# Performance work log

Measured on AMD Instinct MI355X. Metric: run time of the kernel, lower is better.

## Reference

```python
import jax, jax.numpy as jnp
import numpy as np

B, N, C, T = 2048, 512, 64, 128  # batch, codebook size, latent channels, latent time


def setup_inputs() -> dict:
    key = jax.random.key(0)
    k1, k2 = jax.random.split(key)
    y = jax.random.normal(k1, (B, C, T), dtype=jnp.float32)   # encoder latents
    m = jax.random.normal(k2, (N, C, T), dtype=jnp.float32)   # centroid means
    sd = jnp.ones((N, C, T), dtype=jnp.float32)               # centroid variances
    p = jnp.zeros((N,), dtype=jnp.float32) + 1e-6             # cluster counts
    return {"y": y, "m": m, "sd": sd, "p": p}


def reference(y, m, sd, p):
    # --- squared-distance argmin assignment (same math as (y-m)^2 summed over C,T) ---
    b = y.shape[0]
    yf = y.reshape(b, -1)                 # [B, D]
    mf = m.reshape(m.shape[0], -1)        # [N, D]
    d2 = (yf * yf).sum(-1)[:, None] + (mf * mf).sum(-1)[None, :] - 2.0 * (yf @ mf.T)
    assign = jnp.argmin(d2, axis=1)       # [B] int assignments

    # --- sequential, order-sensitive EMA scatter updates (faithful to python loop) ---
    def step(carry, inp):
        p_, m_, sd_ = carry
        yi, zi = inp
        p_ = p_.at[zi].add(1.0)
        mi = m_[zi] * 0.001 + yi * 0.999
        m_ = m_.at[zi].set(mi)
        sdi = (mi - yi) ** 2 * 0.001 + sd_[zi] * 0.999
        sd_ = sd_.at[zi].set(sdi)
        return (p_, m_, sd_), None

    (p, m, sd), _ = jax.lax.scan(step, (p, m, sd), (y, assign))
    return m, sd, p, assign
```

## Files before the change

### kernel.cpp

```cpp
#include <hip/hip_runtime.h>
#include <hip/hip_bf16.h>


#define Bb 2048
#define Nn 512
#define Dd 8192
#define MARGIN 12.0f
#define KC 8
#define KSTEPS 32

typedef __attribute__((ext_vector_type(4))) float f32x4;
typedef __attribute__((ext_vector_type(8))) short s16x8;

__device__ inline unsigned pack2(float lo, float hi) {
    return __builtin_amdgcn_perm(__float_as_uint(hi), __float_as_uint(lo), 0x07060302u);
}

__device__ inline void ema4(float4& mcv, float4& scv, const float4 yv) {
#define EMA_C(c) { mcv.c = mcv.c * 0.001f + yv.c * 0.999f; \
                   float d_ = mcv.c - yv.c;                 \
                   scv.c = d_ * d_ * 0.001f + scv.c * 0.999f; }
    EMA_C(x) EMA_C(y) EMA_C(z) EMA_C(w)
#undef EMA_C
}

__global__ __launch_bounds__(256) void m_norms(const float* __restrict__ M,
                                               float* __restrict__ mm) {
    int n = blockIdx.x, t = threadIdx.x;
    const float4* r = (const float4*)(M + (size_t)n * Dd);
    float s = 0.f;
#pragma unroll
    for (int u = 0; u < 8; u++) {
        float4 v = r[t + 256 * u];
        s += v.x * v.x + v.y * v.y + v.z * v.z + v.w * v.w;
    }
    __shared__ float red[256];
    red[t] = s;
    __syncthreads();
    for (int off = 128; off > 0; off >>= 1) {
        if (t < off) red[t] += red[t + off];
        __syncthreads();
    }
    if (t == 0) mm[n] = red[0];
}

__global__ __launch_bounds__(512, 4) void gemm_coarse(const float* __restrict__ Y,
                                                      const float* __restrict__ M,
                                                      float* __restrict__ part) {
    __shared__ __align__(16) unsigned short As[2][128 * 32];
    __shared__ __align__(16) unsigned short Bs[2][128 * 32];
    const int t = threadIdx.x;
    const int lane = t & 63;
    const int w = t >> 6;

    const int bid = blockIdx.x;
    const int kc = bid & 7;
    const int ct = (bid >> 3) & 3;
    const int rt = bid >> 5;

    const size_t ybase = (size_t)rt * 128 * Dd + (size_t)kc * (KSTEPS * 32);
    const size_t mbase = (size_t)ct * 128 * Dd + (size_t)kc * (KSTEPS * 32);

    const int rowT = t >> 2;
    const int segT = t & 3;
    const int dstOff = rowT * 32 + (segT ^ ((rowT >> 1) & 3)) * 8;
    const float* gA0 = Y + ybase + (size_t)rowT * Dd + segT * 8;
    const float* gB0 = M + mbase + (size_t)rowT * Dd + segT * 8;

    const int wr0 = (w & 3) * 32, wc0 = (w >> 2) * 64;
    const int l15 = lane & 15, quad = lane >> 4;

    f32x4 acc[2][4];
#pragma unroll
    for (int i = 0; i < 2; i++)
#pragma unroll
        for (int j = 0; j < 4; j++) acc[i][j] = (f32x4)(0.0f);

    float4 ra0, ra1, rb0, rb1;
    auto loads = [&](int step) {
        const float* pa = gA0 + step * 32;
        const float* pb = gB0 + step * 32;
        ra0 = *(const float4*)pa;  ra1 = *(const float4*)(pa + 4);
        rb0 = *(const float4*)pb;  rb1 = *(const float4*)(pb + 4);
    };
    auto writes = [&](int buf) {
        union { unsigned u[4]; s16x8 s; } pa_, pb_;
        pa_.u[0] = pack2(ra0.x, ra0.y);  pa_.u[1] = pack2(ra0.z, ra0.w);
        pa_.u[2] = pack2(ra1.x, ra1.y);  pa_.u[3] = pack2(ra1.z, ra1.w);
        pb_.u[0] = pack2(rb0.x, rb0.y);  pb_.u[1] = pack2(rb0.z, rb0.w);
        pb_.u[2] = pack2(rb1.x, rb1.y);  pb_.u[3] = pack2(rb1.z, rb1.w);
        *(s16x8*)(&As[buf][dstOff]) = pa_.s;
        *(s16x8*)(&Bs[buf][dstOff]) = pb_.s;
    };
    auto compute = [&](int buf) {
        s16x8 fa[2], fb[4];
#pragma unroll
        for (int ta = 0; ta < 2; ta++) {
            int rowa = wr0 + ta * 16 + l15;
            int sega = quad ^ ((rowa >> 1) & 3);
            fa[ta] = *(const s16x8*)(&As[buf][rowa * 32 + sega * 8]);
        }
#pragma unroll
        for (int tb = 0; tb < 4; tb++) {
            int rowb = wc0 + tb * 16 + l15;
            int segb = quad ^ ((rowb >> 1) & 3);
            fb[tb] = *(const s16x8*)(&Bs[buf][rowb * 32 + segb * 8]);
        }
#pragma unroll
        for (int i = 0; i < 2; i++)
#pragma unroll
            for (int j = 0; j < 4; j++)
                acc[i][j] = __builtin_amdgcn_mfma_f32_16x16x32_bf16(fa[i], fb[j], acc[i][j], 0, 0, 0);
    };

    loads(0);
    writes(0);
    __syncthreads();
    for (int step = 0; step < KSTEPS; step++) {
        const int buf = step & 1;
        if (step + 1 < KSTEPS) loads(step + 1);
        compute(buf);
        if (step + 1 < KSTEPS) writes(buf ^ 1);
        __syncthreads();
    }

    float* P = part + (size_t)kc * (Bb * Nn);
#pragma unroll
    for (int i = 0; i < 2; i++) {
        int rg = rt * 128 + wr0 + i * 16 + quad * 4;
#pragma unroll
        for (int j = 0; j < 4; j++) {
            int cg = ct * 128 + wc0 + j * 16 + l15;
#pragma unroll
            for (int r = 0; r < 4; r++)
                P[(size_t)(rg + r) * Nn + cg] = acc[i][j][r];
        }
    }
}

__global__ __launch_bounds__(256) void rescore(const float* __restrict__ Y,
                                               const float* __restrict__ M,
                                               const float* __restrict__ part,
                                               const float* __restrict__ mm,
                                               float* __restrict__ assignF) {
    __shared__ float redW[4];
    __shared__ int candList[Nn];
    __shared__ float candD2[Nn];
    __shared__ int candCnt;
    int b = blockIdx.x, t = threadIdx.x, lane = t & 63, w = t >> 6;
    if (t == 0) candCnt = 0;

    int c0 = t, c1 = t + 256;
    float dot0 = 0.f, dot1 = 0.f;
#pragma unroll
    for (int k = 0; k < KC; k++) {
        dot0 += part[(size_t)k * (Bb * Nn) + (size_t)b * Nn + c0];
        dot1 += part[(size_t)k * (Bb * Nn) + (size_t)b * Nn + c1];
    }
    float d0 = mm[c0] - 2.0f * dot0;
    float d1 = mm[c1] - 2.0f * dot1;

    float mn = fminf(d0, d1);
#pragma unroll
    for (int off = 32; off > 0; off >>= 1) mn = fminf(mn, __shfl_xor(mn, off));
    if (lane == 0) redW[w] = mn;
    __syncthreads();
    float thresh = fminf(fminf(redW[0], redW[1]), fminf(redW[2], redW[3])) + MARGIN;

    if (d0 <= thresh) candList[atomicAdd(&candCnt, 1)] = c0;
    if (d1 <= thresh) candList[atomicAdd(&candCnt, 1)] = c1;
    __syncthreads();
    int ncand = candCnt;

    if (ncand == 1) {
        if (t == 0) assignF[b] = (float)candList[0];
        return;
    }

    const float4* yr = (const float4*)(Y + (size_t)b * Dd);
    for (int j = w; j < ncand; j += 4) {
        int c = candList[j];
        const float4* mr = (const float4*)(M + (size_t)c * Dd);
        float p = 0.f;
#pragma unroll 8
        for (int u = 0; u < 32; u++) {
            float4 yv = yr[u * 64 + lane];
            float4 mv = mr[u * 64 + lane];
            p += yv.x * mv.x + yv.y * mv.y + yv.z * mv.z + yv.w * mv.w;
        }
#pragma unroll
        for (int off = 32; off > 0; off >>= 1) p += __shfl_xor(p, off);
        if (lane == 0) candD2[j] = mm[c] - 2.0f * p;
    }
    __syncthreads();

    if (t == 0) {
        float bestV = 3.4e38f;
        int bestI = 0x3fffffff;
        for (int j = 0; j < ncand; j++) {
            float d2e = candD2[j];
            int c = candList[j];
            if (d2e < bestV || (d2e == bestV && c < bestI)) { bestV = d2e; bestI = c; }
        }
        assignF[b] = (float)bestI;
    }
}

__global__ __launch_bounds__(256) void ema_scatter(const float* __restrict__ Y,
                                                   const float* __restrict__ M0,
                                                   const float* __restrict__ SD0,
                                                   const float* __restrict__ P0,
                                                   const float* __restrict__ assignF,
                                                   float* __restrict__ m_out,
                                                   float* __restrict__ sd_out,
                                                   float* __restrict__ p_out) {
    __shared__ int lst[Bb];
    __shared__ int cnt4[4];
    int n = blockIdx.x, s = blockIdx.y, t = threadIdx.x, lane = t & 63, w = t >> 6;

    int eqf[8], myidx[8];
    int cntW = 0;
#pragma unroll
    for (int k = 0; k < 8; k++) {
        int u = w * 8 + k;
        int zi = (int)assignF[u * 64 + lane];
        int eq = (zi == n) ? 1 : 0;
        unsigned long long mask = __ballot(eq != 0);
        eqf[k] = eq;
        myidx[k] = cntW + (int)__popcll(mask & ((1ull << lane) - 1ull));
        cntW += (int)__popcll(mask);
    }
    if (lane == 0) cnt4[w] = cntW;
    __syncthreads();
    int off0 = 0;
#pragma unroll
    for (int q = 0; q < 4; q++) off0 += (q < w) ? cnt4[q] : 0;
    int cnt = cnt4[0] + cnt4[1] + cnt4[2] + cnt4[3];
#pragma unroll
    for (int k = 0; k < 8; k++)
        if (eqf[k]) lst[off0 + myidx[k]] = (w * 8 + k) * 64 + lane;
    if (t == 0 && s == 0) p_out[n] = P0[n] + (float)cnt;
    __syncthreads();

    size_t off = (size_t)n * Dd + (size_t)s * 1024;
    float4 mc = *(const float4*)(M0 + off + 4 * t);
    float4 sc = *(const float4*)(SD0 + off + 4 * t);

    int j = 0;
    for (; j + 16 <= cnt; j += 16) {
        float4 yv[16];
#pragma unroll
        for (int q = 0; q < 16; q++)
            yv[q] = *(const float4*)(Y + (size_t)lst[j + q] * Dd + (size_t)s * 1024 + 4 * t);
#pragma unroll
        for (int q = 0; q < 16; q++) ema4(mc, sc, yv[q]);
    }
    for (; j + 4 <= cnt; j += 4) {
        float4 yv[4];
#pragma unroll
        for (int q = 0; q < 4; q++)
            yv[q] = *(const float4*)(Y + (size_t)lst[j + q] * Dd + (size_t)s * 1024 + 4 * t);
#pragma unroll
        for (int q = 0; q < 4; q++) ema4(mc, sc, yv[q]);
    }
    for (; j < cnt; j++) {
        float4 yv = *(const float4*)(Y + (size_t)lst[j] * Dd + (size_t)s * 1024 + 4 * t);
        ema4(mc, sc, yv);
    }

    *(float4*)(m_out + off + 4 * t) = mc;
    *(float4*)(sd_out + off + 4 * t) = sc;
}

extern "C" void kernel_launch(void* const* d_in, const int* in_sizes, int n_in,
                              void* d_out, int out_size, void* d_ws, size_t ws_size,
                              hipStream_t stream) {
    const float* y  = (const float*)d_in[0];
    const float* m  = (const float*)d_in[1];
    const float* sd = (const float*)d_in[2];
    const float* p  = (const float*)d_in[3];

    float* out     = (float*)d_out;
    float* m_out   = out;
    float* sd_out  = out + 4194304;
    float* p_out   = out + 8388608;
    float* assignF = out + 8389120;
    float* part    = out;

    m_norms    <<<Nn, 256, 0, stream>>>(m, p_out);
    gemm_coarse<<<dim3(512), 512, 0, stream>>>(y, m, part);
    rescore    <<<Bb, 256, 0, stream>>>(y, m, part, p_out, assignF);
    ema_scatter<<<dim3(Nn, 8), 256, 0, stream>>>(y, m, sd, p, assignF, m_out, sd_out, p_out);
}
```

Before: 209.4 us.

## Prefetch two K-steps ahead in coarse GEMM with coalesced row-split loads

The coarse bf16 GEMM now keeps two sets of prefetch registers, so global loads run two K-steps ahead of the MFMA compute instead of one. The global-to-LDS mapping also changes: each thread loads a float4 from two rows 64 apart, giving 128-byte contiguous row segments per 8 threads, and writes 8-byte bf16 stores with no XOR swizzle. The aim is to hide more global latency and improve coalescing. The cost is more registers, possible LDS bank conflicts on the now unswizzled fragment reads, and narrower LDS stores.

```diff
diff --git a/kernel.cpp b/kernel.cpp
--- a/kernel.cpp
+++ b/kernel.cpp
@@ -11,9 +11,17 @@
 
 typedef __attribute__((ext_vector_type(4))) float f32x4;
 typedef __attribute__((ext_vector_type(8))) short s16x8;
+typedef __attribute__((ext_vector_type(2))) unsigned u32x2;
 
 __device__ inline unsigned pack2(float lo, float hi) {
     return __builtin_amdgcn_perm(__float_as_uint(hi), __float_as_uint(lo), 0x07060302u);
+}
+
+__device__ inline void st4bf(unsigned short* dst, const float4 v) {
+    u32x2 x;
+    x[0] = pack2(v.x, v.y);
+    x[1] = pack2(v.z, v.w);
+    *(u32x2*)dst = x;
 }
 
 __device__ inline void ema4(float4& mcv, float4& scv, const float4 yv) {
@@ -61,11 +69,11 @@
     const size_t ybase = (size_t)rt * 128 * Dd + (size_t)kc * (KSTEPS * 32);
     const size_t mbase = (size_t)ct * 128 * Dd + (size_t)kc * (KSTEPS * 32);
 
-    const int rowT = t >> 2;
-    const int segT = t & 3;
-    const int dstOff = rowT * 32 + (segT ^ ((rowT >> 1) & 3)) * 8;
-    const float* gA0 = Y + ybase + (size_t)rowT * Dd + segT * 8;
-    const float* gB0 = M + mbase + (size_t)rowT * Dd + segT * 8;
+    const int rL = t >> 3;
+    const int g4 = (t & 7) * 4;
+    const float* gA0 = Y + ybase + (size_t)rL * Dd + g4;
+    const float* gB0 = M + mbase + (size_t)rL * Dd + g4;
+    const int dst0 = rL * 32 + g4;
 
     const int wr0 = (w & 3) * 32, wc0 = (w >> 2) * 64;
     const int l15 = lane & 15, quad = lane >> 4;
@@ -76,36 +84,42 @@
 #pragma unroll
         for (int j = 0; j < 4; j++) acc[i][j] = (f32x4)(0.0f);
 
-    float4 ra0, ra1, rb0, rb1;
-    auto loads = [&](int step) {
+    float4 aA0, aA1, aB0, aB1;
+    float4 bA0, bA1, bB0, bB1;
+    const size_t rowskip = (size_t)64 * Dd;
+
+    auto loadsA = [&](int step) {
         const float* pa = gA0 + step * 32;
         const float* pb = gB0 + step * 32;
-        ra0 = *(const float4*)pa;  ra1 = *(const float4*)(pa + 4);
-        rb0 = *(const float4*)pb;  rb1 = *(const float4*)(pb + 4);
-    };
-    auto writes = [&](int buf) {
-        union { unsigned u[4]; s16x8 s; } pa_, pb_;
-        pa_.u[0] = pack2(ra0.x, ra0.y);  pa_.u[1] = pack2(ra0.z, ra0.w);
-        pa_.u[2] = pack2(ra1.x, ra1.y);  pa_.u[3] = pack2(ra1.z, ra1.w);
-        pb_.u[0] = pack2(rb0.x, rb0.y);  pb_.u[1] = pack2(rb0.z, rb0.w);
-        pb_.u[2] = pack2(rb1.x, rb1.y);  pb_.u[3] = pack2(rb1.z, rb1.w);
-        *(s16x8*)(&As[buf][dstOff]) = pa_.s;
-        *(s16x8*)(&Bs[buf][dstOff]) = pb_.s;
+        aA0 = *(const float4*)pa;  aA1 = *(const float4*)(pa + rowskip);
+        aB0 = *(const float4*)pb;  aB1 = *(const float4*)(pb + rowskip);
+    };
+    auto loadsB = [&](int step) {
+        const float* pa = gA0 + step * 32;
+        const float* pb = gB0 + step * 32;
+        bA0 = *(const float4*)pa;  bA1 = *(const float4*)(pa + rowskip);
+        bB0 = *(const float4*)pb;  bB1 = *(const float4*)(pb + rowskip);
+    };
+    auto writesA = [&](int buf) {
+        st4bf(&As[buf][dst0],        aA0);
+        st4bf(&As[buf][dst0 + 2048], aA1);
+        st4bf(&Bs[buf][dst0],        aB0);
+        st4bf(&Bs[buf][dst0 + 2048], aB1);
+    };
+    auto writesB = [&](int buf) {
+        st4bf(&As[buf][dst0],        bA0);
+        st4bf(&As[buf][dst0 + 2048], bA1);
+        st4bf(&Bs[buf][dst0],        bB0);
+        st4bf(&Bs[buf][dst0 + 2048], bB1);
     };
     auto compute = [&](int buf) {
         s16x8 fa[2], fb[4];
 #pragma unroll
-        for (int ta = 0; ta < 2; ta++) {
-            int rowa = wr0 + ta * 16 + l15;
-            int sega = quad ^ ((rowa >> 1) & 3);
-            fa[ta] = *(const s16x8*)(&As[buf][rowa * 32 + sega * 8]);
-        }
-#pragma unroll
-        for (int tb = 0; tb < 4; tb++) {
-            int rowb = wc0 + tb * 16 + l15;
-            int segb = quad ^ ((rowb >> 1) & 3);
-            fb[tb] = *(const s16x8*)(&Bs[buf][rowb * 32 + segb * 8]);
-        }
+        for (int ta = 0; ta < 2; ta++)
+            fa[ta] = *(const s16x8*)(&As[buf][(wr0 + ta * 16 + l15) * 32 + quad * 8]);
+#pragma unroll
+        for (int tb = 0; tb < 4; tb++)
+            fb[tb] = *(const s16x8*)(&Bs[buf][(wc0 + tb * 16 + l15) * 32 + quad * 8]);
 #pragma unroll
         for (int i = 0; i < 2; i++)
 #pragma unroll
@@ -113,14 +127,18 @@
                 acc[i][j] = __builtin_amdgcn_mfma_f32_16x16x32_bf16(fa[i], fb[j], acc[i][j], 0, 0, 0);
     };
 
-    loads(0);
-    writes(0);
-    __syncthreads();
-    for (int step = 0; step < KSTEPS; step++) {
-        const int buf = step & 1;
-        if (step + 1 < KSTEPS) loads(step + 1);
-        compute(buf);
-        if (step + 1 < KSTEPS) writes(buf ^ 1);
+    loadsA(0);
+    loadsB(1);
+    writesA(0);
+    __syncthreads();
+    for (int step = 0; step < KSTEPS; step += 2) {
+        if (step + 2 < KSTEPS) loadsA(step + 2);
+        compute(0);
+        writesB(1);
+        __syncthreads();
+        if (step + 3 < KSTEPS) loadsB(step + 3);
+        compute(1);
+        if (step + 2 < KSTEPS) writesA(0);
         __syncthreads();
     }
 
```

Result: no change. 212.7 us (+1.6%).

## Double K tile depth to 64 in coarse GEMM with new swizzle and lighter barrier

Applied to the files above, without the earlier changes.

Doubles the K-slice per pipeline step from 32 to 64 and halves the step count, so each block runs half as many barriers and buffer swaps. Global loads are reorganised into 16-byte chunks across two row halves, stored to LDS as 8-byte bf16 pairs under an XOR swizzle over 8 blocks. __syncthreads is replaced by an explicit lgkmcnt wait plus s_barrier, which skips waiting on outstanding global loads. LDS use doubles to 64KB per block, which may cut occupancy under the 512x4 launch bound, and the narrower LDS stores may raise store instruction count.

```diff
diff --git a/kernel.cpp b/kernel.cpp
--- a/kernel.cpp
+++ b/kernel.cpp
@@ -7,13 +7,22 @@
 #define Dd 8192
 #define MARGIN 12.0f
 #define KC 8
-#define KSTEPS 32
+#define KSTEPS 16
+#define BK 64
 
 typedef __attribute__((ext_vector_type(4))) float f32x4;
 typedef __attribute__((ext_vector_type(8))) short s16x8;
+typedef __attribute__((ext_vector_type(2))) unsigned u32x2;
 
 __device__ inline unsigned pack2(float lo, float hi) {
     return __builtin_amdgcn_perm(__float_as_uint(hi), __float_as_uint(lo), 0x07060302u);
+}
+
+__device__ inline void st4bf(unsigned short* dst, const float4 v) {
+    u32x2 x;
+    x[0] = pack2(v.x, v.y);
+    x[1] = pack2(v.z, v.w);
+    *(u32x2*)dst = x;
 }
 
 __device__ inline void ema4(float4& mcv, float4& scv, const float4 yv) {
@@ -47,8 +56,8 @@
 __global__ __launch_bounds__(512, 4) void gemm_coarse(const float* __restrict__ Y,
                                                       const float* __restrict__ M,
                                                       float* __restrict__ part) {
-    __shared__ __align__(16) unsigned short As[2][128 * 32];
-    __shared__ __align__(16) unsigned short Bs[2][128 * 32];
+    __shared__ __align__(16) unsigned short As[2][128 * BK];
+    __shared__ __align__(16) unsigned short Bs[2][128 * BK];
     const int t = threadIdx.x;
     const int lane = t & 63;
     const int w = t >> 6;
@@ -58,14 +67,16 @@
     const int ct = (bid >> 3) & 3;
     const int rt = bid >> 5;
 
-    const size_t ybase = (size_t)rt * 128 * Dd + (size_t)kc * (KSTEPS * 32);
-    const size_t mbase = (size_t)ct * 128 * Dd + (size_t)kc * (KSTEPS * 32);
-
-    const int rowT = t >> 2;
-    const int segT = t & 3;
-    const int dstOff = rowT * 32 + (segT ^ ((rowT >> 1) & 3)) * 8;
-    const float* gA0 = Y + ybase + (size_t)rowT * Dd + segT * 8;
-    const float* gB0 = M + mbase + (size_t)rowT * Dd + segT * 8;
+    const size_t ybase = (size_t)rt * 128 * Dd + (size_t)kc * (KSTEPS * BK);
+    const size_t mbase = (size_t)ct * 128 * Dd + (size_t)kc * (KSTEPS * BK);
+
+    const int rL = t >> 3;
+    const int c8 = t & 7;
+    const float* gA0 = Y + ybase + (size_t)rL * Dd + c8 * 4;
+    const float* gB0 = M + mbase + (size_t)rL * Dd + c8 * 4;
+    const int swz = rL & 7;
+    const int dA0 = rL * BK + ((((c8 >> 1) + 0) ^ swz) << 3) + (c8 & 1) * 4;
+    const int dA1 = rL * BK + ((((c8 >> 1) + 4) ^ swz) << 3) + (c8 & 1) * 4;
 
     const int wr0 = (w & 3) * 32, wc0 = (w >> 2) * 64;
     const int l15 = lane & 15, quad = lane >> 4;
@@ -76,53 +87,68 @@
 #pragma unroll
         for (int j = 0; j < 4; j++) acc[i][j] = (f32x4)(0.0f);
 
-    float4 ra0, ra1, rb0, rb1;
+    float4 rA00, rA01, rA10, rA11;
+    float4 rB00, rB01, rB10, rB11;
+    const size_t rowskip = (size_t)64 * Dd;
+
     auto loads = [&](int step) {
-        const float* pa = gA0 + step * 32;
-        const float* pb = gB0 + step * 32;
-        ra0 = *(const float4*)pa;  ra1 = *(const float4*)(pa + 4);
-        rb0 = *(const float4*)pb;  rb1 = *(const float4*)(pb + 4);
+        const float* pa = gA0 + step * BK;
+        const float* pb = gB0 + step * BK;
+        rA00 = *(const float4*)pa;             rA01 = *(const float4*)(pa + 32);
+        rA10 = *(const float4*)(pa + rowskip); rA11 = *(const float4*)(pa + rowskip + 32);
+        rB00 = *(const float4*)pb;             rB01 = *(const float4*)(pb + 32);
+        rB10 = *(const float4*)(pb + rowskip); rB11 = *(const float4*)(pb + rowskip + 32);
     };
     auto writes = [&](int buf) {
-        union { unsigned u[4]; s16x8 s; } pa_, pb_;
-        pa_.u[0] = pack2(ra0.x, ra0.y);  pa_.u[1] = pack2(ra0.z, ra0.w);
-        pa_.u[2] = pack2(ra1.x, ra1.y);  pa_.u[3] = pack2(ra1.z, ra1.w);
-        pb_.u[0] = pack2(rb0.x, rb0.y);  pb_.u[1] = pack2(rb0.z, rb0.w);
-        pb_.u[2] = pack2(rb1.x, rb1.y);  pb_.u[3] = pack2(rb1.z, rb1.w);
-        *(s16x8*)(&As[buf][dstOff]) = pa_.s;
-        *(s16x8*)(&Bs[buf][dstOff]) = pb_.s;
+        st4bf(&As[buf][dA0],            rA00);
+        st4bf(&As[buf][dA1],            rA01);
+        st4bf(&As[buf][dA0 + 64 * BK],  rA10);
+        st4bf(&As[buf][dA1 + 64 * BK],  rA11);
+        st4bf(&Bs[buf][dA0],            rB00);
+        st4bf(&Bs[buf][dA1],            rB01);
+        st4bf(&Bs[buf][dA0 + 64 * BK],  rB10);
+        st4bf(&Bs[buf][dA1 + 64 * BK],  rB11);
     };
     auto compute = [&](int buf) {
-        s16x8 fa[2], fb[4];
-#pragma unroll
-        for (int ta = 0; ta < 2; ta++) {
-            int rowa = wr0 + ta * 16 + l15;
-            int sega = quad ^ ((rowa >> 1) & 3);
-            fa[ta] = *(const s16x8*)(&As[buf][rowa * 32 + sega * 8]);
+#pragma unroll
+        for (int ks = 0; ks < 2; ks++) {
+            s16x8 fa[2], fb[4];
+#pragma unroll
+            for (int ta = 0; ta < 2; ta++) {
+                int row = wr0 + ta * 16 + l15;
+                int blk = (ks * 4 + quad) ^ (row & 7);
+                fa[ta] = *(const s16x8*)(&As[buf][row * BK + (blk << 3)]);
+            }
+#pragma unroll
+            for (int tb = 0; tb < 4; tb++) {
+                int row = wc0 + tb * 16 + l15;
+                int blk = (ks * 4 + quad) ^ (row & 7);
+                fb[tb] = *(const s16x8*)(&Bs[buf][row * BK + (blk << 3)]);
+            }
+#pragma unroll
+            for (int i = 0; i < 2; i++)
+#pragma unroll
+                for (int j = 0; j < 4; j++)
+                    acc[i][j] = __builtin_amdgcn_mfma_f32_16x16x32_bf16(fa[i], fb[j], acc[i][j], 0, 0, 0);
         }
-#pragma unroll
-        for (int tb = 0; tb < 4; tb++) {
-            int rowb = wc0 + tb * 16 + l15;
-            int segb = quad ^ ((rowb >> 1) & 3);
-            fb[tb] = *(const s16x8*)(&Bs[buf][rowb * 32 + segb * 8]);
-        }
-#pragma unroll
-        for (int i = 0; i < 2; i++)
-#pragma unroll
-            for (int j = 0; j < 4; j++)
-                acc[i][j] = __builtin_amdgcn_mfma_f32_16x16x32_bf16(fa[i], fb[j], acc[i][j], 0, 0, 0);
     };
+
+#define BARRIER() do {                                          \
+        asm volatile("s_waitcnt lgkmcnt(0)" ::: "memory");      \
+        __builtin_amdgcn_s_barrier();                           \
+    } while (0)
 
     loads(0);
     writes(0);
-    __syncthreads();
+    BARRIER();
     for (int step = 0; step < KSTEPS; step++) {
         const int buf = step & 1;
         if (step + 1 < KSTEPS) loads(step + 1);
         compute(buf);
         if (step + 1 < KSTEPS) writes(buf ^ 1);
-        __syncthreads();
-    }
+        BARRIER();
+    }
+#undef BARRIER
 
     float* P = part + (size_t)kc * (Bb * Nn);
 #pragma unroll
```

Measured after the change: 212.3 us. Within noise of the previous version (+1.4%).
